# Optimization experiments

Measured on AMD Instinct MI355X. Metric: run time of the kernel, lower is better.

Reference implementation:

```python
import jax, jax.numpy as jnp
import numpy as np

BATCH = 256
SEQ_LEN = 96
PRED_LEN = 96
ENC_IN = 321
D_MODEL = 512


def setup_inputs() -> dict:
    key = jax.random.key(0)
    ks = jax.random.split(key, 7)
    s = 1.0 / np.sqrt(D_MODEL)
    x_enc = jax.random.normal(ks[0], (BATCH, SEQ_LEN, ENC_IN), jnp.float32)
    Wih = jax.random.uniform(ks[1], (4 * D_MODEL, ENC_IN), jnp.float32, -s, s)
    Whh = jax.random.uniform(ks[2], (4 * D_MODEL, D_MODEL), jnp.float32, -s, s)
    bih = jax.random.uniform(ks[3], (4 * D_MODEL,), jnp.float32, -s, s)
    bhh = jax.random.uniform(ks[4], (4 * D_MODEL,), jnp.float32, -s, s)
    Wp = jax.random.uniform(ks[5], (ENC_IN, D_MODEL), jnp.float32, -s, s)
    bp = jax.random.uniform(ks[6], (ENC_IN,), jnp.float32, -s, s)
    return {"x_enc": x_enc, "Wih": Wih, "Whh": Whh, "bih": bih, "bhh": bhh, "Wp": Wp, "bp": bp}


def _lstm_step(h, c, xt, Wih, Whh, bih, bhh):
    # PyTorch LSTM gate layout: [i, f, g, o]
    g = xt @ Wih.T + h @ Whh.T + (bih + bhh)  # (B, 4*D)
    i, f, gg, o = jnp.split(g, 4, axis=-1)
    c = jax.nn.sigmoid(f) * c + jax.nn.sigmoid(i) * jnp.tanh(gg)
    h = jax.nn.sigmoid(o) * jnp.tanh(c)
    return h, c


def reference(x_enc, Wih, Whh, bih, bhh, Wp, bp):
    # Instance norm over time (use_norm=True); means detached as in torch
    means = jax.lax.stop_gradient(jnp.mean(x_enc, axis=1, keepdims=True))
    xc = x_enc - means
    stdev = jnp.sqrt(jnp.var(xc, axis=1, keepdims=True) + 1e-5)
    x = xc / stdev

    B = x.shape[0]
    h0 = jnp.zeros((B, D_MODEL), x.dtype)
    c0 = jnp.zeros((B, D_MODEL), x.dtype)

    def enc_step(carry, xt):
        h, c = carry
        h, c = _lstm_step(h, c, xt, Wih, Whh, bih, bhh)
        return (h, c), None

    (h, c), _ = jax.lax.scan(enc_step, (h0, c0), jnp.swapaxes(x, 0, 1))

    def dec_step(carry, _):
        h, c = carry
        y = h @ Wp.T + bp          # (B, ENC_IN) decoded from hidden
        h, c = _lstm_step(h, c, y, Wih, Whh, bih, bhh)
        return (h, c), y

    _, ys = jax.lax.scan(dec_step, (h, c), None, length=PRED_LEN)
    dec_out = jnp.swapaxes(ys, 0, 1)  # (B, PRED_LEN, ENC_IN)

    dec_out = dec_out * stdev[:, 0:1, :] + means[:, 0:1, :]
    return dec_out
```

## Files before the change

### kernel.cpp

```cpp
#include <hip/hip_runtime.h>
#include <hip/hip_bf16.h>
#include <math.h>

#define BB 256
#define TT 96
#define PP 96
#define CC 321
#define CP 352
#define DD 512
#define GG 2048
#define NSTEPS 191
#define HROT ((size_t)BB * DD)

typedef __attribute__((ext_vector_type(8))) short bf16x8;
typedef __attribute__((ext_vector_type(4))) float f32x4;
typedef __hip_bfloat16 bf16;
typedef unsigned long long u64;

__global__ void norm_kernel(const float* __restrict__ x, float* __restrict__ meanp,
                            float* __restrict__ stdp, bf16* __restrict__ xn) {
    int g = blockIdx.x * 256 + threadIdx.x;
    if (g >= BB * CC) return;
    int b = g / CC, c = g % CC;
    const float* xp = x + b * TT * CC + c;
    float s = 0.f;
    for (int t = 0; t < TT; ++t) s += xp[t * CC];
    float mu = s * (1.f / TT);
    float v = 0.f;
    for (int t = 0; t < TT; ++t) { float d0 = xp[t * CC] - mu; v += d0 * d0; }
    float sd = sqrtf(v * (1.f / TT) + 1e-5f);
    float rs = 1.f / sd;
    meanp[g] = mu;
    stdp[g] = sd;
    for (int t = 0; t < TT; ++t)
        xn[(t * BB + b) * CP + c] = __float2bfloat16((xp[t * CC] - mu) * rs);
}

__global__ void cast_pad_kernel(const float* __restrict__ src, bf16* __restrict__ dst,
                                int rows, int cols, int ldd) {
    int i = blockIdx.x * 256 + threadIdx.x;
    if (i >= rows * cols) return;
    int r = i / cols, c = i % cols;
    dst[r * ldd + c] = __float2bfloat16(src[i]);
}

__global__ void transpose_wp_kernel(const float* __restrict__ wp, bf16* __restrict__ wpt) {
    int i = blockIdx.x * 256 + threadIdx.x;
    if (i >= DD * CC) return;
    int d = i / CC, c = i % CC;
    wpt[d * CP + c] = __float2bfloat16(wp[c * DD + d]);
}

__global__ void bias_kernel(const float* __restrict__ Wih, const float* __restrict__ bih,
                            const float* __restrict__ bhh, const float* __restrict__ bp,
                            float* __restrict__ bsum, float* __restrict__ beff) {
    int j = blockIdx.x * 256 + threadIdx.x;
    if (j >= GG) return;
    float s = bih[j] + bhh[j];
    float acc = 0.f;
    const float* w = Wih + j * CC;
    for (int c = 0; c < CC; ++c) acc += w[c] * bp[c];
    bsum[j] = s;
    beff[j] = s + acc;
}

__device__ __forceinline__ void gemm_core_64x64(const bf16* A, int lda, const bf16* Bt,
                                                int ldb, int K, int m0, int n0,
                                                f32x4 acc[4]) {
    __shared__ unsigned short As[64][40];
    __shared__ unsigned short Bs[64][40];
    int tid = threadIdx.x;
    int w = tid >> 6, lane = tid & 63;
    int quad = lane >> 4, col = lane & 15;
    int lr = tid >> 2, lc = (tid & 3) * 8;
    for (int k0 = 0; k0 < K; k0 += 32) {
        __syncthreads();
        *(uint4*)&As[lr][lc] = *(const uint4*)&A[(size_t)(m0 + lr) * lda + k0 + lc];
        *(uint4*)&Bs[lr][lc] = *(const uint4*)&Bt[(size_t)(n0 + lr) * ldb + k0 + lc];
        __syncthreads();
        bf16x8 a = *(const bf16x8*)&As[w * 16 + col][quad * 8];
#pragma unroll
        for (int nt = 0; nt < 4; ++nt) {
            bf16x8 bfr = *(const bf16x8*)&Bs[nt * 16 + col][quad * 8];
            acc[nt] = __builtin_amdgcn_mfma_f32_16x16x32_bf16(a, bfr, acc[nt], 0, 0, 0);
        }
    }
}

__global__ void weff_kernel(const bf16* __restrict__ WihP, const bf16* __restrict__ WpTP,
                            const float* __restrict__ Whh, bf16* __restrict__ WeffP) {
    f32x4 acc[4] = {{0,0,0,0},{0,0,0,0},{0,0,0,0},{0,0,0,0}};
    int m0 = blockIdx.y * 64, n0 = blockIdx.x * 64;
    gemm_core_64x64(WihP, CP, WpTP, CP, CP, m0, n0, acc);
    int tid = threadIdx.x, w = tid >> 6, lane = tid & 63;
    int quad = lane >> 4, col = lane & 15;
#pragma unroll
    for (int nt = 0; nt < 4; ++nt)
#pragma unroll
        for (int r = 0; r < 4; ++r) {
            int j = m0 + w * 16 + quad * 4 + r;
            int d = n0 + nt * 16 + col;
            WeffP[j * DD + d] = __float2bfloat16(acc[nt][r] + Whh[j * DD + d]);
        }
}

__global__ void proj_kernel(const bf16* __restrict__ Hd, const bf16* __restrict__ WpP,
                            const float* __restrict__ bp, const float* __restrict__ stdp,
                            const float* __restrict__ meanp, float* __restrict__ out) {
    f32x4 acc[4] = {{0,0,0,0},{0,0,0,0},{0,0,0,0},{0,0,0,0}};
    int m0 = blockIdx.x * 64, n0 = blockIdx.y * 64;
    gemm_core_64x64(Hd, DD, WpP, DD, DD, m0, n0, acc);
    int tid = threadIdx.x, w = tid >> 6, lane = tid & 63;
    int quad = lane >> 4, col = lane & 15;
#pragma unroll
    for (int nt = 0; nt < 4; ++nt) {
        int c = n0 + nt * 16 + col;
        if (c >= CC) continue;
        float bpc = bp[c];
#pragma unroll
        for (int r = 0; r < 4; ++r) {
            int row = m0 + w * 16 + quad * 4 + r;
            int t = row >> 8, b = row & 255;
            float y = acc[nt][r] + bpc;
            int sc = b * CC + c;
            out[(b * PP + t) * CC + c] = y * stdp[sc] + meanp[sc];
        }
    }
}

__global__ __launch_bounds__(128, 1) void lstm_persistent(
        const bf16* __restrict__ xn,
        const bf16* __restrict__ WihP,
        const bf16* __restrict__ WhhP,
        const bf16* __restrict__ WeffP,
        const float* __restrict__ bsum, const float* __restrict__ beff,
        bf16* __restrict__ Hall,
        unsigned int* __restrict__ bar) {
    __shared__ unsigned short Whs[4 * 16 * 64 * 8];
    __shared__ unsigned short Wxs[4 * 11 * 64 * 8];
    __shared__ int role_sh;

    const int tid = threadIdx.x;
    const int w = tid >> 6, lane = tid & 63;
    const int quad = lane >> 4, col = lane & 15;

    unsigned int xcd;
    asm volatile("s_getreg_b32 %0, hwreg(HW_REG_XCC_ID)" : "=s"(xcd));
    xcd &= 7;
    if (tid == 0)
        role_sh = (int)__hip_atomic_fetch_add(&bar[xcd], 1u, __ATOMIC_RELAXED,
                                              __HIP_MEMORY_SCOPE_AGENT);
    __syncthreads();
    const int dt = role_sh & 31;
    const int bt = (int)xcd;
    const int d0 = dt * 16;
    const int b0 = bt * 32;
    const int batch = b0 + w * 16 + col;
    unsigned int* const flags = bar + 64 + bt * 64;

    for (int i = tid; i < 4096; i += 128) {
        int q = i & 3, ki = (i >> 2) & 15, row = (i >> 6) & 15, gt = i >> 10;
        *(uint4*)&Whs[((gt * 16 + ki) * 64 + q * 16 + row) * 8] =
            *(const uint4*)&WhhP[(size_t)(gt * DD + d0 + row) * DD + ki * 32 + q * 8];
    }
    for (int i = tid; i < 2816; i += 128) {
        int q = i & 3; int t = i >> 2; int ki = t % 11; t /= 11;
        int row = t & 15, gt = t >> 4;
        *(uint4*)&Wxs[((gt * 11 + ki) * 64 + q * 16 + row) * 8] =
            *(const uint4*)&WihP[(size_t)(gt * DD + d0 + row) * CP + ki * 32 + q * 8];
    }
    __syncthreads();

    float creg[4] = {0.f, 0.f, 0.f, 0.f};
    float bs_[16], be_[16];
#pragma unroll
    for (int g4 = 0; g4 < 16; ++g4) {
        int gt = g4 >> 2, r = g4 & 3;
        bs_[g4] = bsum[gt * DD + d0 + quad * 4 + r];
        be_[g4] = beff[gt * DD + d0 + quad * 4 + r];
    }

    const size_t own_slot = (size_t)batch * DD + d0 + quad * 4;
    const int fidx = (lane & 31) * 2 + w;

    for (int s = 0; s < NSTEPS; ++s) {
        const bool enc = (s < TT);
        bf16* h_out = Hall + (size_t)s * HROT;

        f32x4 acc[4] = {{0,0,0,0},{0,0,0,0},{0,0,0,0},{0,0,0,0}};

        if (enc) {
            uint4 xf[11];
            const uint4* xp = (const uint4*)(xn + (size_t)(s * BB + batch) * CP) + quad;
#pragma unroll
            for (int ki = 0; ki < 11; ++ki) xf[ki] = xp[ki * 4];
#pragma unroll
            for (int ki = 0; ki < 11; ++ki) {
                bf16x8 xv = *(bf16x8*)&xf[ki];
#pragma unroll
                for (int gt = 0; gt < 4; ++gt) {
                    bf16x8 wf = *(const bf16x8*)&Wxs[((gt * 11 + ki) * 64 + lane) * 8];
                    acc[gt] = __builtin_amdgcn_mfma_f32_16x16x32_bf16(wf, xv, acc[gt], 0, 0, 0);
                }
            }
        }

        if (s > 0) {
            unsigned int tgt = (unsigned int)s;
            int guard = 0;
            while (__hip_atomic_load(&flags[fidx], __ATOMIC_RELAXED,
                                     __HIP_MEMORY_SCOPE_AGENT) < tgt) {
                __builtin_amdgcn_s_sleep(2);
                if (++guard >= (1 << 20)) break;
            }
            __builtin_amdgcn_sched_barrier(0);
        }

        if (s == TT) {
            __syncthreads();
            for (int i = tid; i < 4096; i += 128) {
                int q = i & 3, ki = (i >> 2) & 15, row = (i >> 6) & 15, gt = i >> 10;
                *(uint4*)&Whs[((gt * 16 + ki) * 64 + q * 16 + row) * 8] =
                    *(const uint4*)&WeffP[(size_t)(gt * DD + d0 + row) * DD + ki * 32 + q * 8];
            }
            __syncthreads();
        }

        if (s > 0) {
            uint4 hq[16];
            const uint4* hp = (const uint4*)(Hall + (size_t)(s - 1) * HROT
                                             + (size_t)batch * DD) + quad;
#pragma unroll
            for (int ki = 0; ki < 16; ++ki) hq[ki] = hp[ki * 4];
#pragma unroll
            for (int ki = 0; ki < 16; ++ki) {
                bf16x8 hv = *(bf16x8*)&hq[ki];
#pragma unroll
                for (int gt = 0; gt < 4; ++gt) {
                    bf16x8 wf = *(const bf16x8*)&Whs[((gt * 16 + ki) * 64 + lane) * 8];
                    acc[gt] = __builtin_amdgcn_mfma_f32_16x16x32_bf16(wf, hv, acc[gt], 0, 0, 0);
                }
            }
        }

        u64 pack = 0;
#pragma unroll
        for (int r = 0; r < 4; ++r) {
            float iv = acc[0][r] + (enc ? bs_[0 + r] : be_[0 + r]);
            float fv = acc[1][r] + (enc ? bs_[4 + r] : be_[4 + r]);
            float gv = acc[2][r] + (enc ? bs_[8 + r] : be_[8 + r]);
            float ov = acc[3][r] + (enc ? bs_[12 + r] : be_[12 + r]);
            float si = 1.f / (1.f + __expf(-iv));
            float sf = 1.f / (1.f + __expf(-fv));
            float so = 1.f / (1.f + __expf(-ov));
            float tg = tanhf(gv);
            float cc = sf * creg[r] + si * tg;
            creg[r] = cc;
            float hvv = so * tanhf(cc);
            union { bf16 h; unsigned short u; } cv;
            cv.h = __float2bfloat16(hvv);
            pack |= (u64)cv.u << (16 * r);
        }
        __hip_atomic_store((u64*)&h_out[own_slot], pack,
                           __ATOMIC_RELAXED, __HIP_MEMORY_SCOPE_AGENT);
        asm volatile("s_waitcnt vmcnt(0)" ::: "memory");
        if (lane == 0)
            __hip_atomic_store(&flags[dt * 2 + w], (unsigned int)(s + 1),
                               __ATOMIC_RELAXED, __HIP_MEMORY_SCOPE_AGENT);
    }
}

extern "C" void kernel_launch(void* const* d_in, const int* in_sizes, int n_in,
                              void* d_out, int out_size, void* d_ws, size_t ws_size,
                              hipStream_t stream) {
    (void)in_sizes; (void)n_in; (void)out_size;
    const float* x_enc = (const float*)d_in[0];
    const float* Wih   = (const float*)d_in[1];
    const float* Whh   = (const float*)d_in[2];
    const float* bih   = (const float*)d_in[3];
    const float* bhh   = (const float*)d_in[4];
    const float* Wp    = (const float*)d_in[5];
    const float* bp    = (const float*)d_in[6];
    float* out = (float*)d_out;

    char* ws = (char*)d_ws;
    size_t off = 0;
    float* meanp = (float*)(ws + off); off += (size_t)BB * CC * 4;
    float* stdp  = (float*)(ws + off); off += (size_t)BB * CC * 4;
    bf16* xnormP = (bf16*)(ws + off);  off += (size_t)TT * BB * CP * 2;
    bf16* WihP   = (bf16*)(ws + off);  off += (size_t)GG * CP * 2;
    bf16* WhhP   = (bf16*)(ws + off);  off += (size_t)GG * DD * 2;
    bf16* WeffP  = (bf16*)(ws + off);  off += (size_t)GG * DD * 2;
    bf16* WpTP   = (bf16*)(ws + off);  off += (size_t)DD * CP * 2;
    bf16* WpP    = (bf16*)(ws + off);  off += (size_t)384 * DD * 2;
    float* bsum  = (float*)(ws + off); off += (size_t)GG * 4;
    float* beff  = (float*)(ws + off); off += (size_t)GG * 4;
    bf16* Hall   = (bf16*)(ws + off);  off += (size_t)NSTEPS * HROT * 2;
    unsigned int* bar = (unsigned int*)(ws + off); off += 4096;
    if (ws_size < off) return;

    hipMemsetAsync(xnormP, 0, (size_t)TT * BB * CP * 2, stream);
    hipMemsetAsync(WihP,   0, (size_t)GG * CP * 2, stream);
    hipMemsetAsync(WpTP,   0, (size_t)DD * CP * 2, stream);
    hipMemsetAsync(WpP,    0, (size_t)384 * DD * 2, stream);
    hipMemsetAsync(bar,    0, 4096, stream);

    norm_kernel<<<(BB * CC + 255) / 256, 256, 0, stream>>>(x_enc, meanp, stdp, xnormP);
    cast_pad_kernel<<<(GG * CC + 255) / 256, 256, 0, stream>>>(Wih, WihP, GG, CC, CP);
    cast_pad_kernel<<<(GG * DD + 255) / 256, 256, 0, stream>>>(Whh, WhhP, GG, DD, DD);
    cast_pad_kernel<<<(CC * DD + 255) / 256, 256, 0, stream>>>(Wp, WpP, CC, DD, DD);
    transpose_wp_kernel<<<(DD * CC + 255) / 256, 256, 0, stream>>>(Wp, WpTP);
    bias_kernel<<<GG / 256, 256, 0, stream>>>(Wih, bih, bhh, bp, bsum, beff);
    weff_kernel<<<dim3(DD / 64, GG / 64), 256, 0, stream>>>(WihP, WpTP, Whh, WeffP);

    const bf16* xn_c = xnormP;  const bf16* wih_c = WihP;
    const bf16* whh_c = WhhP;   const bf16* weff_c = WeffP;
    const float* bs_c = bsum;   const float* be_c = beff;
    bf16* ha_c = Hall; unsigned int* bar_c = bar;
    void* args[] = {&xn_c, &wih_c, &whh_c, &weff_c, &bs_c, &be_c,
                    &ha_c, &bar_c};
    hipLaunchCooperativeKernel((void*)lstm_persistent, dim3(256), dim3(128),
                               args, 0, stream);

    proj_kernel<<<dim3(PP * BB / 64, 384 / 64), 256, 0, stream>>>(
        Hall + 95 * HROT, WpP, bp, stdp, meanp, out);
}
```

Before: 1.462 ms.

## Fuse output projection into persistent LSTM and switch to counter-based group barrier

Removes the separate projection GEMM kernel and computes each decoder output inside the persistent LSTM kernel. Each of the first 24 column tiles multiplies its already-loaded hidden state by a projection slice kept in LDS, then writes the denormalized output. The per-wave flag array is replaced by one per-XCD atomic counter barrier with a block-level syncthreads. The projection work overlaps the barrier wait but lengthens the critical path of some blocks, and the single counter concentrates atomic contention.

```diff
diff --git a/kernel.cpp b/kernel.cpp
--- a/kernel.cpp
+++ b/kernel.cpp
@@ -104,30 +104,6 @@
         }
 }
 
-__global__ void proj_kernel(const bf16* __restrict__ Hd, const bf16* __restrict__ WpP,
-                            const float* __restrict__ bp, const float* __restrict__ stdp,
-                            const float* __restrict__ meanp, float* __restrict__ out) {
-    f32x4 acc[4] = {{0,0,0,0},{0,0,0,0},{0,0,0,0},{0,0,0,0}};
-    int m0 = blockIdx.x * 64, n0 = blockIdx.y * 64;
-    gemm_core_64x64(Hd, DD, WpP, DD, DD, m0, n0, acc);
-    int tid = threadIdx.x, w = tid >> 6, lane = tid & 63;
-    int quad = lane >> 4, col = lane & 15;
-#pragma unroll
-    for (int nt = 0; nt < 4; ++nt) {
-        int c = n0 + nt * 16 + col;
-        if (c >= CC) continue;
-        float bpc = bp[c];
-#pragma unroll
-        for (int r = 0; r < 4; ++r) {
-            int row = m0 + w * 16 + quad * 4 + r;
-            int t = row >> 8, b = row & 255;
-            float y = acc[nt][r] + bpc;
-            int sc = b * CC + c;
-            out[(b * PP + t) * CC + c] = y * stdp[sc] + meanp[sc];
-        }
-    }
-}
-
 __global__ __launch_bounds__(128, 1) void lstm_persistent(
         const bf16* __restrict__ xn,
         const bf16* __restrict__ WihP,
@@ -135,9 +111,14 @@
         const bf16* __restrict__ WeffP,
         const float* __restrict__ bsum, const float* __restrict__ beff,
         bf16* __restrict__ Hall,
+        const bf16* __restrict__ WpP,
+        const float* __restrict__ bp,
+        const float* __restrict__ stdp, const float* __restrict__ meanp,
+        float* __restrict__ out,
         unsigned int* __restrict__ bar) {
     __shared__ unsigned short Whs[4 * 16 * 64 * 8];
     __shared__ unsigned short Wxs[4 * 11 * 64 * 8];
+    __shared__ unsigned short PAs[16 * 64 * 8];
     __shared__ int role_sh;
 
     const int tid = threadIdx.x;
@@ -156,7 +137,7 @@
     const int d0 = dt * 16;
     const int b0 = bt * 32;
     const int batch = b0 + w * 16 + col;
-    unsigned int* const flags = bar + 64 + bt * 64;
+    unsigned int* const ctr = bar + 256 + bt * 32;
 
     for (int i = tid; i < 4096; i += 128) {
         int q = i & 3, ki = (i >> 2) & 15, row = (i >> 6) & 15, gt = i >> 10;
@@ -169,6 +150,15 @@
         *(uint4*)&Wxs[((gt * 11 + ki) * 64 + q * 16 + row) * 8] =
             *(const uint4*)&WihP[(size_t)(gt * DD + d0 + row) * CP + ki * 32 + q * 8];
     }
+    const bool pact = (dt < 24);
+    const int c0 = dt * 16;
+    if (pact) {
+        for (int i = tid; i < 1024; i += 128) {
+            int q = i & 3, ki = (i >> 2) & 15, row = (i >> 6) & 15;
+            *(uint4*)&PAs[(ki * 64 + q * 16 + row) * 8] =
+                *(const uint4*)&WpP[(size_t)(c0 + row) * DD + ki * 32 + q * 8];
+        }
+    }
     __syncthreads();
 
     float creg[4] = {0.f, 0.f, 0.f, 0.f};
@@ -179,13 +169,32 @@
         bs_[g4] = bsum[gt * DD + d0 + quad * 4 + r];
         be_[g4] = beff[gt * DD + d0 + quad * 4 + r];
     }
+    float pbp[4], pstd[4], pmean[4];
+    bool pok[4];
+#pragma unroll
+    for (int r = 0; r < 4; ++r) {
+        int c = c0 + quad * 4 + r;
+        pok[r] = pact && (c < CC);
+        pbp[r]   = pok[r] ? bp[c] : 0.f;
+        pstd[r]  = pok[r] ? stdp[batch * CC + c] : 0.f;
+        pmean[r] = pok[r] ? meanp[batch * CC + c] : 0.f;
+    }
 
     const size_t own_slot = (size_t)batch * DD + d0 + quad * 4;
-    const int fidx = (lane & 31) * 2 + w;
+    unsigned int gen = 0;
 
     for (int s = 0; s < NSTEPS; ++s) {
         const bool enc = (s < TT);
         bf16* h_out = Hall + (size_t)s * HROT;
+
+        if (s == TT) {
+            for (int i = tid; i < 4096; i += 128) {
+                int q = i & 3, ki = (i >> 2) & 15, row = (i >> 6) & 15, gt = i >> 10;
+                *(uint4*)&Whs[((gt * 16 + ki) * 64 + q * 16 + row) * 8] =
+                    *(const uint4*)&WeffP[(size_t)(gt * DD + d0 + row) * DD + ki * 32 + q * 8];
+            }
+            __syncthreads();
+        }
 
         f32x4 acc[4] = {{0,0,0,0},{0,0,0,0},{0,0,0,0},{0,0,0,0}};
 
@@ -205,29 +214,8 @@
             }
         }
 
+        uint4 hq[16];
         if (s > 0) {
-            unsigned int tgt = (unsigned int)s;
-            int guard = 0;
-            while (__hip_atomic_load(&flags[fidx], __ATOMIC_RELAXED,
-                                     __HIP_MEMORY_SCOPE_AGENT) < tgt) {
-                __builtin_amdgcn_s_sleep(2);
-                if (++guard >= (1 << 20)) break;
-            }
-            __builtin_amdgcn_sched_barrier(0);
-        }
-
-        if (s == TT) {
-            __syncthreads();
-            for (int i = tid; i < 4096; i += 128) {
-                int q = i & 3, ki = (i >> 2) & 15, row = (i >> 6) & 15, gt = i >> 10;
-                *(uint4*)&Whs[((gt * 16 + ki) * 64 + q * 16 + row) * 8] =
-                    *(const uint4*)&WeffP[(size_t)(gt * DD + d0 + row) * DD + ki * 32 + q * 8];
-            }
-            __syncthreads();
-        }
-
-        if (s > 0) {
-            uint4 hq[16];
             const uint4* hp = (const uint4*)(Hall + (size_t)(s - 1) * HROT
                                              + (size_t)batch * DD) + quad;
 #pragma unroll
@@ -264,9 +252,58 @@
         __hip_atomic_store((u64*)&h_out[own_slot], pack,
                            __ATOMIC_RELAXED, __HIP_MEMORY_SCOPE_AGENT);
         asm volatile("s_waitcnt vmcnt(0)" ::: "memory");
-        if (lane == 0)
-            __hip_atomic_store(&flags[dt * 2 + w], (unsigned int)(s + 1),
-                               __ATOMIC_RELAXED, __HIP_MEMORY_SCOPE_AGENT);
+        __syncthreads();
+        ++gen;
+        if (tid == 0)
+            __hip_atomic_fetch_add(ctr, 1u, __ATOMIC_RELAXED,
+                                   __HIP_MEMORY_SCOPE_AGENT);
+
+        if (pact && s >= TT) {
+            f32x4 pacc = {0.f, 0.f, 0.f, 0.f};
+#pragma unroll
+            for (int ki = 0; ki < 16; ++ki) {
+                bf16x8 pa = *(const bf16x8*)&PAs[(ki * 64 + lane) * 8];
+                bf16x8 hv = *(bf16x8*)&hq[ki];
+                pacc = __builtin_amdgcn_mfma_f32_16x16x32_bf16(pa, hv, pacc, 0, 0, 0);
+            }
+            int t = s - TT;
+#pragma unroll
+            for (int r = 0; r < 4; ++r)
+                if (pok[r])
+                    out[((size_t)batch * PP + t) * CC + c0 + quad * 4 + r] =
+                        (pacc[r] + pbp[r]) * pstd[r] + pmean[r];
+        }
+
+        if (tid == 0) {
+            unsigned int tgt = gen * 32u;
+            int guard = 0;
+            while (__hip_atomic_load(ctr, __ATOMIC_RELAXED,
+                                     __HIP_MEMORY_SCOPE_AGENT) < tgt) {
+                __builtin_amdgcn_s_sleep(1);
+                if (++guard >= (1 << 20)) break;
+            }
+        }
+        __syncthreads();
+    }
+
+    if (pact) {
+        uint4 hq[16];
+        const uint4* hp = (const uint4*)(Hall + (size_t)(NSTEPS - 1) * HROT
+                                         + (size_t)batch * DD) + quad;
+#pragma unroll
+        for (int ki = 0; ki < 16; ++ki) hq[ki] = hp[ki * 4];
+        f32x4 pacc = {0.f, 0.f, 0.f, 0.f};
+#pragma unroll
+        for (int ki = 0; ki < 16; ++ki) {
+            bf16x8 pa = *(const bf16x8*)&PAs[(ki * 64 + lane) * 8];
+            bf16x8 hv = *(bf16x8*)&hq[ki];
+            pacc = __builtin_amdgcn_mfma_f32_16x16x32_bf16(pa, hv, pacc, 0, 0, 0);
+        }
+#pragma unroll
+        for (int r = 0; r < 4; ++r)
+            if (pok[r])
+                out[((size_t)batch * PP + (PP - 1)) * CC + c0 + quad * 4 + r] =
+                    (pacc[r] + pbp[r]) * pstd[r] + pmean[r];
     }
 }
 
@@ -316,12 +353,12 @@
     const bf16* xn_c = xnormP;  const bf16* wih_c = WihP;
     const bf16* whh_c = WhhP;   const bf16* weff_c = WeffP;
     const float* bs_c = bsum;   const float* be_c = beff;
-    bf16* ha_c = Hall; unsigned int* bar_c = bar;
+    bf16* ha_c = Hall;          const bf16* wp_c = WpP;
+    const float* bp_c = bp;     const float* sd_c = stdp;
+    const float* mn_c = meanp;  float* out_c = out;
+    unsigned int* bar_c = bar;
     void* args[] = {&xn_c, &wih_c, &whh_c, &weff_c, &bs_c, &be_c,
-                    &ha_c, &bar_c};
+                    &ha_c, &wp_c, &bp_c, &sd_c, &mn_c, &out_c, &bar_c};
     hipLaunchCooperativeKernel((void*)lstm_persistent, dim3(256), dim3(128),
                                args, 0, stream);
-
-    proj_kernel<<<dim3(PP * BB / 64, 384 / 64), 256, 0, stream>>>(
-        Hall + 95 * HROT, WpP, bp, stdp, meanp, out);
-}
+}
```

After: 1.309 ms. 10.5% less time.
